# Kernel tuning notes

Measured on AMD Instinct MI355X. Metric: run time of the kernel, lower is better.

## Reference

```python
import jax, jax.numpy as jnp
import numpy as np

B, IN, O, F, FH = 512, 2000, 64, 8, 32
D = 64 + FH * O  # 2112


def setup_inputs() -> dict:
    key = jax.random.key(0)
    ks = jax.random.split(key, 17)
    rn = lambda k, s: jax.random.normal(k, s, dtype=jnp.float32) * 0.05
    return dict(
        x=rn(ks[0], (B, IN)),
        fc_in_W=rn(ks[1], (1024, IN)), fc_in_b=rn(ks[2], (1024,)),
        fc1_W=rn(ks[3], (128, 1024)), fc1_b=rn(ks[4], (128,)),
        out1_W=rn(ks[5], (O, 64, 128)), out1_b=rn(ks[6], (O, 64)),
        coef_nn_W=rn(ks[7], (F, FH, 1)), coef_nn_b=rn(ks[8], (F, FH)),
        coef_att_W=rn(ks[9], (F, FH, FH)),
        out_att_W=rn(ks[10], (O, FH, FH)),
        nodes_trans_W=rn(ks[11], (O, O)),
        trans_gcn_W=rn(ks[12], (D, D)),
        outmap_W=rn(ks[13], (1, D)), outmap_b=rn(ks[14], (1,)),
        prelu_a=jnp.float32(0.25),
        coef_m=rn(ks[15], (O, O, F)),
    )


def reference(x, fc_in_W, fc_in_b, fc1_W, fc1_b, out1_W, out1_b,
              coef_nn_W, coef_nn_b, coef_att_W, out_att_W,
              nodes_trans_W, trans_gcn_W, outmap_W, outmap_b, prelu_a, coef_m):
    elu = jax.nn.elu
    # trunk MLP
    h = jax.nn.relu(x @ fc_in_W.T + fc_in_b)          # [B,1024]
    h = jax.nn.relu(h @ fc1_W.T + fc1_b)              # [B,128]
    # per-output-node heads (vectorized over the output_dim loop)
    hiddens = jax.nn.relu(jnp.einsum('bk,odk->bod', h, out1_W) + out1_b)  # [B,O,64]
    # per-feature coef embedding: Linear(1,FH) on each coef_m[:,:,i] slice
    cf = elu(coef_m[..., None] * coef_nn_W[:, :, 0] + coef_nn_b)          # [O,O,F,FH]
    # sum over concatenated feature axis (F*FH) of exp(elu(.))
    s = jnp.exp(elu(cf)).sum(axis=(2, 3))[:, :, None, None]               # [O,O,1,1]
    lin = jnp.einsum('xyfh,fgh->xyfg', cf, coef_att_W)                    # per-feature attention linear
    p = elu(jnp.exp(elu(cf)) * lin / s)
    cfs = elu(p.sum(axis=2) / F)                                          # [O,O,FH]
    # node-level attention (vectorized over the output_dim loop)
    coef_sum = jnp.exp(elu(cfs)).sum(axis=1)                              # [O,FH]
    p2 = jnp.exp(elu(cfs)) / coef_sum[:, None, :]                         # [O,O,FH]
    lin2 = jnp.einsum('oih,igh->oig', cfs, out_att_W)
    att = (p2 * lin2).reshape(O, O * FH)                                  # concat over i (i-major)
    hc = jnp.concatenate(
        [hiddens, jnp.broadcast_to(att[None], (x.shape[0], O, O * FH))], axis=2)  # [B,O,D]
    nt = jnp.einsum('bpd,op->bod', hc, nodes_trans_W)                     # node mixing Linear(O,O)
    trans = jax.nn.sigmoid(jnp.einsum('bod,ed->boe', nt, trans_gcn_W))    # [B,O,D]
    z = (trans @ outmap_W.T + outmap_b).squeeze(-1)                       # [B,O]
    return jnp.where(z >= 0, z, prelu_a * z)                              # PReLU
```

## Files before the change

kernel.cpp:

```cpp
#include <hip/hip_runtime.h>
#include <math.h>

typedef __attribute__((ext_vector_type(8))) short bf16x8;
typedef __attribute__((ext_vector_type(4))) float f32x4;

static __device__ __forceinline__ float fast_elu(float x) {
    return x > 0.0f ? x : __expf(x) - 1.0f;
}

static __device__ __forceinline__ unsigned short f2bf(float f) {
    unsigned int u = __float_as_uint(f);
    unsigned int r = (u + 0x7FFFu + ((u >> 16) & 1u)) >> 16;
    return (unsigned short)r;
}

static __device__ __forceinline__ bf16x8 cvt8(const float* __restrict__ s) {
    float4 a = *reinterpret_cast<const float4*>(s);
    float4 b = *reinterpret_cast<const float4*>(s + 4);
    bf16x8 r;
    r[0] = (short)f2bf(a.x); r[1] = (short)f2bf(a.y);
    r[2] = (short)f2bf(a.z); r[3] = (short)f2bf(a.w);
    r[4] = (short)f2bf(b.x); r[5] = (short)f2bf(b.y);
    r[6] = (short)f2bf(b.z); r[7] = (short)f2bf(b.w);
    return r;
}

#define T0 16384
#define T1 16896
#define T2 82432
#define T3 99328
#define CONV_BLOCKS 388

static __device__ __forceinline__ void conv_phase(
    int bx,
    const float* __restrict__ fc1W, const float* __restrict__ ntW,
    const float* __restrict__ out1W, const float* __restrict__ tgw,
    unsigned short* __restrict__ fc1Wb, unsigned short* __restrict__ Wb,
    unsigned short* __restrict__ out1WbT, unsigned short* __restrict__ Gb)
{
    int u = bx * 256 + threadIdx.x;
    if (u < T0) {
        int i8 = u * 8;
        *reinterpret_cast<bf16x8*>(&fc1Wb[i8]) = cvt8(&fc1W[i8]);
    } else if (u < T1) {
        int i8 = (u - T0) * 8;
        *reinterpret_cast<bf16x8*>(&Wb[i8]) = cvt8(&ntW[i8]);
    } else if (u < T2) {
        int i = u - T1;
        int n = i >> 4, kc = i & 15;
        int d = n >> 6, p = n & 63;
        *reinterpret_cast<bf16x8*>(&out1WbT[(size_t)n * 128 + kc * 8]) =
            cvt8(&out1W[(size_t)((p << 6) | d) * 128 + kc * 8]);
    } else if (u < T3) {
        int i = u - T2;
        int e = i >> 3, c = i & 7;
        *reinterpret_cast<bf16x8*>(&Gb[(size_t)e * 64 + c * 8]) =
            cvt8(&tgw[(size_t)e * 2112 + c * 8]);
    }
}

static __device__ __forceinline__ void coef_phase(
    int bx, float* __restrict__ smemf,
    const float* __restrict__ coef_m, const float* __restrict__ cW,
    const float* __restrict__ cB, const float* __restrict__ attW,
    float* __restrict__ cfs)
{
    float* cf_s = smemf;
    float* part = smemf + 1024;
    const int t = threadIdx.x;
    const int wv = t >> 6, lane = t & 63;
    const int xy = bx * 4 + wv;
    float ls = 0.0f;
    #pragma unroll
    for (int i = 0; i < 4; ++i) {
        int idx = i * 64 + lane;
        int f = idx >> 5;
        float v = fast_elu(coef_m[xy * 8 + f] * cW[idx] + cB[idx]);
        cf_s[wv * 256 + idx] = v;
        ls += __expf(fast_elu(v));
    }
    #pragma unroll
    for (int m = 1; m < 64; m <<= 1) ls += __shfl_xor(ls, m, 64);
    __syncthreads();
    const float rs = __builtin_amdgcn_rcpf(ls);
    const int g = lane & 31, fg = lane >> 5;
    float acc = 0.0f;
    for (int f = fg * 4; f < fg * 4 + 4; ++f) {
        float lin = 0.0f;
        #pragma unroll
        for (int h = 0; h < 32; h += 4) {
            float4 Lv = *reinterpret_cast<const float4*>(&cf_s[wv * 256 + f * 32 + h]);
            float4 Wv = *reinterpret_cast<const float4*>(&attW[f * 1024 + g * 32 + h]);
            lin += Lv.x * Wv.x + Lv.y * Wv.y + Lv.z * Wv.z + Lv.w * Wv.w;
        }
        float e = __expf(fast_elu(cf_s[wv * 256 + f * 32 + g]));
        acc += fast_elu(e * lin * rs);
    }
    part[wv * 64 + lane] = acc;
    __syncthreads();
    if (lane < 32) {
        float tot = part[wv * 64 + lane] + part[wv * 64 + lane + 32];
        cfs[xy * 32 + lane] = fast_elu(tot * 0.125f);
    }
}

static __device__ __forceinline__ void att_phase(
    int o, int ic, float* __restrict__ smemf,
    const float* __restrict__ cfs, const float* __restrict__ oattW,
    float* __restrict__ att)
{
    float* L    = smemf;
    float* red  = smemf + 2048;
    float* csum = smemf + 2304;
    const int t = threadIdx.x;
    #pragma unroll
    for (int j = 0; j < 8; ++j) L[t + 256 * j] = cfs[o * 2048 + t + 256 * j];
    __syncthreads();
    {
        int h = t & 31, ig = t >> 5;
        float ps = 0.0f;
        for (int i = ig * 8; i < ig * 8 + 8; ++i) ps += __expf(fast_elu(L[i * 32 + h]));
        red[t] = ps;
        __syncthreads();
        if (t < 32) {
            float cs = 0.0f;
            #pragma unroll
            for (int j = 0; j < 8; ++j) cs += red[j * 32 + t];
            csum[t] = cs;
        }
        __syncthreads();
    }
    int idx = ic * 256 + t;
    int i = idx >> 5, g = idx & 31;
    float lin2 = 0.0f;
    #pragma unroll
    for (int h = 0; h < 32; h += 4) {
        float4 Lv = *reinterpret_cast<const float4*>(&L[i * 32 + h]);
        float4 Wv = *reinterpret_cast<const float4*>(&oattW[i * 1024 + g * 32 + h]);
        lin2 += Lv.x * Wv.x + Lv.y * Wv.y + Lv.z * Wv.z + Lv.w * Wv.w;
    }
    float p2 = __expf(fast_elu(L[idx])) * __builtin_amdgcn_rcpf(csum[g]);
    att[o * 2048 + idx] = p2 * lin2;
}

static __device__ __forceinline__ void natt_phase(
    int bx, float* __restrict__ smemf,
    const float* __restrict__ ntW, const float* __restrict__ att,
    unsigned short* __restrict__ nattb)
{
    float* ntW_s = smemf;
    float* att_s = smemf + 64 * 65;
    const int t = threadIdx.x;
    const int d0 = bx * 16;
    #pragma unroll
    for (int j = 0; j < 16; ++j) {
        int idx = t + 256 * j;
        ntW_s[(idx >> 6) * 65 + (idx & 63)] = ntW[idx];
    }
    #pragma unroll
    for (int j = 0; j < 4; ++j) {
        int idx = t + 256 * j;
        int p = idx >> 4, dd = idx & 15;
        att_s[p * 17 + dd] = att[p * 2048 + d0 + dd];
    }
    __syncthreads();
    const int dd = t & 15, ob = (t >> 4) * 4;
    float acc[4] = {0.0f, 0.0f, 0.0f, 0.0f};
    for (int p = 0; p < 64; ++p) {
        float av = att_s[p * 17 + dd];
        #pragma unroll
        for (int i = 0; i < 4; ++i) acc[i] += ntW_s[(ob + i) * 65 + p] * av;
    }
    #pragma unroll
    for (int i = 0; i < 4; ++i)
        nattb[(ob + i) * 2048 + d0 + dd] = f2bf(acc[i]);
}

static __device__ __forceinline__ void gemm_core(
    const unsigned short* __restrict__ A, int lda,
    const unsigned short* __restrict__ B, int ldb,
    float* __restrict__ C, int ldc, long strideCz,
    int kchunk, int bn, int bm, int bz,
    unsigned short* __restrict__ As, unsigned short* __restrict__ Bs)
{
    const int t = threadIdx.x;
    const int w = t >> 6, lane = t & 63, l16 = lane & 15, quad = lane >> 4;
    const int n0 = bn * 64, m0 = bm * 64;
    const int kb0 = bz * kchunk;
    const int r = t >> 2, koff = (t & 3) * 8;
    C += (size_t)bz * strideCz;

    const size_t arow = (size_t)(m0 + r) * lda + koff;
    const size_t brow = (size_t)(n0 + r) * ldb + koff;
    bf16x8 av = *reinterpret_cast<const bf16x8*>(&A[arow + kb0]);
    bf16x8 bv = *reinterpret_cast<const bf16x8*>(&B[brow + kb0]);

    f32x4 acc[4] = {};
    for (int kb = kb0; kb < kb0 + kchunk; kb += 32) {
        __syncthreads();
        *reinterpret_cast<bf16x8*>(&As[r * 40 + koff]) = av;
        *reinterpret_cast<bf16x8*>(&Bs[r * 40 + koff]) = bv;
        if (kb + 32 < kb0 + kchunk) {
            av = *reinterpret_cast<const bf16x8*>(&A[arow + kb + 32]);
            bv = *reinterpret_cast<const bf16x8*>(&B[brow + kb + 32]);
        }
        __syncthreads();
        bf16x8 af = *reinterpret_cast<const bf16x8*>(&As[(w * 16 + l16) * 40 + quad * 8]);
        #pragma unroll
        for (int nt = 0; nt < 4; ++nt) {
            bf16x8 bf = *reinterpret_cast<const bf16x8*>(&Bs[(nt * 16 + l16) * 40 + quad * 8]);
            acc[nt] = __builtin_amdgcn_mfma_f32_16x16x32_bf16(af, bf, acc[nt], 0, 0, 0);
        }
    }
    #pragma unroll
    for (int nt = 0; nt < 4; ++nt)
        #pragma unroll
        for (int i = 0; i < 4; ++i) {
            int m = m0 + w * 16 + quad * 4 + i;
            int n = n0 + nt * 16 + l16;
            C[(size_t)m * ldc + n] = acc[nt][i];
        }
}

static __device__ __forceinline__ void gemm_xf_core(
    const float* __restrict__ A, const float* __restrict__ B,
    const float* __restrict__ bias, unsigned short* __restrict__ Cb,
    int bn, int bm,
    unsigned short* __restrict__ As, unsigned short* __restrict__ Bs)
{
    const int t = threadIdx.x;
    const int w = t >> 6, lane = t & 63, l16 = lane & 15, quad = lane >> 4;
    const int n0 = bn * 64, m0 = bm * 64;
    const int r = t >> 2, koff = (t & 3) * 8;

    const float* arow = A + (size_t)(m0 + r) * 2000;
    const float* brow = B + (size_t)(n0 + r) * 2000;
    const bf16x8 zv = {0, 0, 0, 0, 0, 0, 0, 0};

    bf16x8 av = (koff < 2000) ? cvt8(arow + koff) : zv;
    bf16x8 bv = (koff < 2000) ? cvt8(brow + koff) : zv;

    f32x4 acc[4] = {};
    for (int kb = 0; kb < 2000; kb += 32) {
        __syncthreads();
        *reinterpret_cast<bf16x8*>(&As[r * 40 + koff]) = av;
        *reinterpret_cast<bf16x8*>(&Bs[r * 40 + koff]) = bv;
        if (kb + 32 < 2000) {
            int k = kb + 32 + koff;
            av = (k < 2000) ? cvt8(arow + k) : zv;
            bv = (k < 2000) ? cvt8(brow + k) : zv;
        }
        __syncthreads();
        bf16x8 af = *reinterpret_cast<const bf16x8*>(&As[(w * 16 + l16) * 40 + quad * 8]);
        #pragma unroll
        for (int nt = 0; nt < 4; ++nt) {
            bf16x8 bf = *reinterpret_cast<const bf16x8*>(&Bs[(nt * 16 + l16) * 40 + quad * 8]);
            acc[nt] = __builtin_amdgcn_mfma_f32_16x16x32_bf16(af, bf, acc[nt], 0, 0, 0);
        }
    }
    #pragma unroll
    for (int nt = 0; nt < 4; ++nt)
        #pragma unroll
        for (int i = 0; i < 4; ++i) {
            int m = m0 + w * 16 + quad * 4 + i;
            int n = n0 + nt * 16 + l16;
            float v = acc[nt][i] + bias[n];
            v = fmaxf(v, 0.0f);
            Cb[(size_t)m * 1024 + n] = f2bf(v);
        }
}

static __device__ __forceinline__ void gemm_tgwa_core(
    const float* __restrict__ tgw,
    const unsigned short* __restrict__ B,
    float* __restrict__ C, long strideCz,
    int kchunk, int bm, int bz,
    unsigned short* __restrict__ As, unsigned short* __restrict__ Bs)
{
    const int t = threadIdx.x;
    const int w = t >> 6, lane = t & 63, l16 = lane & 15, quad = lane >> 4;
    const int m0 = bm * 64;
    const int kb0 = bz * kchunk;
    const int r = t >> 2, koff = (t & 3) * 8;
    C += (size_t)bz * strideCz;

    const float* arow = tgw + (size_t)(m0 + r) * 2112 + 64 + koff;
    const unsigned short* brow = B + (size_t)r * 2048 + koff;
    bf16x8 av = cvt8(arow + kb0);
    bf16x8 bv = *reinterpret_cast<const bf16x8*>(brow + kb0);

    f32x4 acc[4] = {};
    for (int kb = kb0; kb < kb0 + kchunk; kb += 32) {
        __syncthreads();
        *reinterpret_cast<bf16x8*>(&As[r * 40 + koff]) = av;
        *reinterpret_cast<bf16x8*>(&Bs[r * 40 + koff]) = bv;
        if (kb + 32 < kb0 + kchunk) {
            av = cvt8(arow + kb + 32);
            bv = *reinterpret_cast<const bf16x8*>(brow + kb + 32);
        }
        __syncthreads();
        bf16x8 af = *reinterpret_cast<const bf16x8*>(&As[(w * 16 + l16) * 40 + quad * 8]);
        #pragma unroll
        for (int nt = 0; nt < 4; ++nt) {
            bf16x8 bf = *reinterpret_cast<const bf16x8*>(&Bs[(nt * 16 + l16) * 40 + quad * 8]);
            acc[nt] = __builtin_amdgcn_mfma_f32_16x16x32_bf16(af, bf, acc[nt], 0, 0, 0);
        }
    }
    #pragma unroll
    for (int nt = 0; nt < 4; ++nt)
        #pragma unroll
        for (int i = 0; i < 4; ++i) {
            int m = m0 + w * 16 + quad * 4 + i;
            int n = nt * 16 + l16;
            C[(size_t)m * 64 + n] = acc[nt][i];
        }
}

static __device__ __forceinline__ void gemm_fa_core(
    const float* __restrict__ Ap, int lda, long apstride, int nparts,
    const float* __restrict__ abias,
    const unsigned short* __restrict__ B, int ldb,
    unsigned short* __restrict__ Cb, int ldc,
    const float* __restrict__ bias,
    int kchunk, int bn, int bm,
    unsigned short* __restrict__ As, unsigned short* __restrict__ Bs)
{
    const int t = threadIdx.x;
    const int w = t >> 6, lane = t & 63, l16 = lane & 15, quad = lane >> 4;
    const int n0 = bn * 64, m0 = bm * 64;
    const int r = t >> 2, koff = (t & 3) * 8;

    f32x4 acc[4] = {};
    for (int kb = 0; kb < kchunk; kb += 32) {
        float a8[8];
        {
            const float* base = &Ap[(size_t)(m0 + r) * lda + kb + koff];
            float4 s0 = *reinterpret_cast<const float4*>(base);
            float4 s1 = *reinterpret_cast<const float4*>(base + 4);
            for (int j = 1; j < nparts; ++j) {
                const float* pj = base + (size_t)j * apstride;
                float4 p0 = *reinterpret_cast<const float4*>(pj);
                float4 p1 = *reinterpret_cast<const float4*>(pj + 4);
                s0.x += p0.x; s0.y += p0.y; s0.z += p0.z; s0.w += p0.w;
                s1.x += p1.x; s1.y += p1.y; s1.z += p1.z; s1.w += p1.w;
            }
            float4 b0 = *reinterpret_cast<const float4*>(&abias[kb + koff]);
            float4 b1 = *reinterpret_cast<const float4*>(&abias[kb + koff + 4]);
            a8[0] = fmaxf(s0.x + b0.x, 0.0f); a8[1] = fmaxf(s0.y + b0.y, 0.0f);
            a8[2] = fmaxf(s0.z + b0.z, 0.0f); a8[3] = fmaxf(s0.w + b0.w, 0.0f);
            a8[4] = fmaxf(s1.x + b1.x, 0.0f); a8[5] = fmaxf(s1.y + b1.y, 0.0f);
            a8[6] = fmaxf(s1.z + b1.z, 0.0f); a8[7] = fmaxf(s1.w + b1.w, 0.0f);
        }
        bf16x8 bv = *reinterpret_cast<const bf16x8*>(&B[(size_t)(n0 + r) * ldb + kb + koff]);
        __syncthreads();
        ushort4 lo, hi;
        lo.x = f2bf(a8[0]); lo.y = f2bf(a8[1]); lo.z = f2bf(a8[2]); lo.w = f2bf(a8[3]);
        hi.x = f2bf(a8[4]); hi.y = f2bf(a8[5]); hi.z = f2bf(a8[6]); hi.w = f2bf(a8[7]);
        *reinterpret_cast<ushort4*>(&As[r * 40 + koff]) = lo;
        *reinterpret_cast<ushort4*>(&As[r * 40 + koff + 4]) = hi;
        *reinterpret_cast<bf16x8*>(&Bs[r * 40 + koff]) = bv;
        __syncthreads();
        bf16x8 af = *reinterpret_cast<const bf16x8*>(&As[(w * 16 + l16) * 40 + quad * 8]);
        #pragma unroll
        for (int nt = 0; nt < 4; ++nt) {
            bf16x8 bf = *reinterpret_cast<const bf16x8*>(&Bs[(nt * 16 + l16) * 40 + quad * 8]);
            acc[nt] = __builtin_amdgcn_mfma_f32_16x16x32_bf16(af, bf, acc[nt], 0, 0, 0);
        }
    }
    #pragma unroll
    for (int nt = 0; nt < 4; ++nt)
        #pragma unroll
        for (int i = 0; i < 4; ++i) {
            int m = m0 + w * 16 + quad * 4 + i;
            int n = n0 + nt * 16 + l16;
            int bidx = (((n & 63) << 6) | (n >> 6));
            float v = acc[nt][i] + bias[bidx];
            v = fmaxf(v, 0.0f);
            Cb[(size_t)m * ldc + n] = f2bf(v);
        }
}

static __device__ __forceinline__ void nt1f_phase(
    int b, unsigned short* __restrict__ smemu,
    const unsigned short* __restrict__ hbT, const unsigned short* __restrict__ Wb,
    unsigned short* __restrict__ nt1b)
{
    unsigned short* HtT   = smemu;
    unsigned short* nt1_s = smemu + 64 * 72;
    const int t = threadIdx.x;
    const int w = t >> 6, lane = t & 63, l16 = lane & 15, quad = lane >> 4;

    const unsigned short* src = hbT + (size_t)b * 4096;
    #pragma unroll
    for (int j = 0; j < 2; ++j) {
        int c = t + j * 256;
        *reinterpret_cast<bf16x8*>(&HtT[(c >> 3) * 72 + (c & 7) * 8]) =
            *reinterpret_cast<const bf16x8*>(&src[c * 8]);
    }
    __syncthreads();

    bf16x8 aW[2];
    #pragma unroll
    for (int h = 0; h < 2; ++h)
        aW[h] = *reinterpret_cast<const bf16x8*>(&Wb[(w * 16 + l16) * 64 + h * 32 + quad * 8]);
    #pragma unroll
    for (int dt = 0; dt < 4; ++dt) {
        f32x4 acc = {0.0f, 0.0f, 0.0f, 0.0f};
        #pragma unroll
        for (int h = 0; h < 2; ++h) {
            bf16x8 bf = *reinterpret_cast<const bf16x8*>(
                &HtT[(dt * 16 + l16) * 72 + h * 32 + quad * 8]);
            acc = __builtin_amdgcn_mfma_f32_16x16x32_bf16(aW[h], bf, acc, 0, 0, 0);
        }
        #pragma unroll
        for (int i = 0; i < 4; ++i)
            nt1_s[(w * 16 + quad * 4 + i) * 72 + dt * 16 + l16] = f2bf(acc[i]);
    }
    __syncthreads();
    #pragma unroll
    for (int j = 0; j < 2; ++j) {
        int c = t + j * 256;
        *reinterpret_cast<bf16x8*>(&nt1b[(size_t)b * 4096 + c * 8]) =
            *reinterpret_cast<const bf16x8*>(&nt1_s[(c >> 3) * 72 + (c & 7) * 8]);
    }
}

__global__ __launch_bounds__(256) void uber1(
    const float* fc1W, const float* ntW, const float* out1W, const float* tgw,
    unsigned short* fc1Wb, unsigned short* Wb, unsigned short* out1WbT,
    unsigned short* Gb,
    const float* coef_m, const float* cW, const float* cB, const float* attW,
    float* cfs)
{
    __shared__ __align__(16) float smemf[1280];
    int bx = blockIdx.x;
    if (bx < CONV_BLOCKS)
        conv_phase(bx, fc1W, ntW, out1W, tgw, fc1Wb, Wb, out1WbT, Gb);
    else
        coef_phase(bx - CONV_BLOCKS, smemf, coef_m, cW, cB, attW, cfs);
}

__global__ __launch_bounds__(256) void uber2(
    const float* x, const float* fcinW, const float* fc_in_b,
    unsigned short* h1b,
    const float* cfs, const float* oattW, float* att)
{
    __shared__ __align__(16) float smemf[2592];
    int bx = blockIdx.x;
    if (bx < 128) {
        unsigned short* As = (unsigned short*)smemf;
        gemm_xf_core(x, fcinW, fc_in_b, h1b, bx & 15, bx >> 4, As, As + 2560);
    } else {
        int b2 = bx - 128;
        att_phase(b2 & 63, b2 >> 6, smemf, cfs, oattW, att);
    }
}

__global__ __launch_bounds__(256) void uber3(
    const unsigned short* h1b, const unsigned short* fc1Wb, float* h2p,
    const float* ntW, const float* att, unsigned short* nattb)
{
    __shared__ __align__(16) float smemf[5248];
    int bx = blockIdx.x;
    if (bx < 64) {
        unsigned short* As = (unsigned short*)smemf;
        gemm_core(h1b, 1024, fc1Wb, 1024, h2p, 128, 65536L,
                  256, bx & 1, (bx >> 1) & 7, bx >> 4, As, As + 2560);
    } else {
        natt_phase(bx - 64, smemf, ntW, att, nattb);
    }
}

__global__ __launch_bounds__(256) void uber4(
    const float* h2p, const float* fc1_b, const unsigned short* out1WbT,
    unsigned short* hbT, const float* out1_b,
    const float* tgw, const unsigned short* nattb, float* cpT)
{
    __shared__ __align__(16) float smemf[2560];
    unsigned short* As = (unsigned short*)smemf;
    int bx = blockIdx.x;
    if (bx < 512) {
        gemm_fa_core(h2p, 128, 65536L, 4, fc1_b, out1WbT, 128,
                     hbT, 4096, out1_b, 128, bx & 63, bx >> 6, As, As + 2560);
    } else {
        int b2 = bx - 512;
        gemm_tgwa_core(tgw, nattb, cpT, 135168L, 256,
                       b2 % 33, b2 / 33, As, As + 2560);
    }
}

__global__ __launch_bounds__(256) void uber5(
    const unsigned short* hbT, const unsigned short* Wb, unsigned short* nt1b,
    const float* cpT, float* cmatT)
{
    __shared__ __align__(16) unsigned short smemu[2 * 64 * 72];
    int bx = blockIdx.x;
    if (bx < 512) {
        nt1f_phase(bx, smemu, hbT, Wb, nt1b);
    } else {
        int i = (bx - 512) * 256 + threadIdx.x;
        if (i < 135168) {
            float a = 0.0f;
            #pragma unroll
            for (int j = 0; j < 8; ++j) a += cpT[i + (long)j * 135168L];
            cmatT[i] = a;
        }
    }
}

__global__ __launch_bounds__(256) void final_nb(
    const unsigned short* __restrict__ nt1b,
    const unsigned short* __restrict__ Gb,
    const float* __restrict__ cmatT,
    const float* __restrict__ outW,
    float* __restrict__ zpart)
{
    const int t = threadIdx.x;
    const int w = t >> 6, lane = t & 63, l16 = lane & 15, quad = lane >> 4;
    const int eb = blockIdx.x;
    const int b0 = blockIdx.y * 16;
    const int o = w * 16 + l16;

    bf16x8 ga[4][2];
    float cm[4][4], wv[4][4];
    #pragma unroll
    for (int et = 0; et < 4; ++et) {
        #pragma unroll
        for (int h = 0; h < 2; ++h)
            ga[et][h] = *reinterpret_cast<const bf16x8*>(
                &Gb[(size_t)(eb * 64 + et * 16 + l16) * 64 + h * 32 + quad * 8]);
        #pragma unroll
        for (int i = 0; i < 4; ++i) {
            int e = eb * 64 + et * 16 + quad * 4 + i;
            cm[et][i] = cmatT[(size_t)e * 64 + o];
            wv[et][i] = outW[e];
        }
    }

    const unsigned short* bbase = nt1b + (size_t)b0 * 4096 + o * 64 + quad * 8;
    bf16x8 bf0 = *reinterpret_cast<const bf16x8*>(bbase);
    bf16x8 bf1 = *reinterpret_cast<const bf16x8*>(bbase + 32);

    for (int bi = 0; bi < 16; ++bi) {
        bf16x8 nb0, nb1;
        if (bi < 15) {
            nb0 = *reinterpret_cast<const bf16x8*>(bbase + (size_t)(bi + 1) * 4096);
            nb1 = *reinterpret_cast<const bf16x8*>(bbase + (size_t)(bi + 1) * 4096 + 32);
        }
        float zo = 0.0f;
        #pragma unroll
        for (int et = 0; et < 4; ++et) {
            f32x4 acc = {cm[et][0], cm[et][1], cm[et][2], cm[et][3]};
            acc = __builtin_amdgcn_mfma_f32_16x16x32_bf16(ga[et][0], bf0, acc, 0, 0, 0);
            acc = __builtin_amdgcn_mfma_f32_16x16x32_bf16(ga[et][1], bf1, acc, 0, 0, 0);
            #pragma unroll
            for (int i = 0; i < 4; ++i)
                zo += __builtin_amdgcn_rcpf(1.0f + __expf(-acc[i])) * wv[et][i];
        }
        zo += __shfl_xor(zo, 16, 64);
        zo += __shfl_xor(zo, 32, 64);
        if (quad == 0)
            zpart[((size_t)eb * 512 + b0 + bi) * 64 + o] = zo;
        bf0 = nb0; bf1 = nb1;
    }
}

__global__ __launch_bounds__(256) void finish_kernel(
    const float* __restrict__ zpart, const float* __restrict__ outB,
    const float* __restrict__ preluA, float* __restrict__ out)
{
    int i = blockIdx.x * 256 + threadIdx.x;
    float z = 0.0f;
    for (int j = 0; j < 33; ++j) z += zpart[(size_t)j * 32768 + i];
    z += outB[0];
    float pa = preluA[0];
    out[i] = (z >= 0.0f) ? z : pa * z;
}

extern "C" void kernel_launch(void* const* d_in, const int* in_sizes, int n_in,
                              void* d_out, int out_size, void* d_ws, size_t ws_size,
                              hipStream_t stream)
{
    const float* x       = (const float*)d_in[0];
    const float* fc_in_W = (const float*)d_in[1];
    const float* fc_in_b = (const float*)d_in[2];
    const float* fc1_W   = (const float*)d_in[3];
    const float* fc1_b   = (const float*)d_in[4];
    const float* out1_W  = (const float*)d_in[5];
    const float* out1_b  = (const float*)d_in[6];
    const float* cW      = (const float*)d_in[7];
    const float* cB      = (const float*)d_in[8];
    const float* cattW   = (const float*)d_in[9];
    const float* oattW   = (const float*)d_in[10];
    const float* ntW     = (const float*)d_in[11];
    const float* tgw     = (const float*)d_in[12];
    const float* outW    = (const float*)d_in[13];
    const float* outB    = (const float*)d_in[14];
    const float* preluA  = (const float*)d_in[15];
    const float* coef_m  = (const float*)d_in[16];
    float* out = (float*)d_out;
    float* ws  = (float*)d_ws;

    unsigned short* fc1Wb   = (unsigned short*)(ws + 0);
    unsigned short* Wb      = (unsigned short*)(ws + 65536);
    unsigned short* out1WbT = (unsigned short*)(ws + 67584);
    unsigned short* Gb      = (unsigned short*)(ws + 329728);
    float*          cfs     = ws + 397312;
    float*          att     = ws + 528384;
    unsigned short* nattb   = (unsigned short*)(ws + 659456);
    unsigned short* h1b     = (unsigned short*)(ws + 724992);
    float*          h2p     = ws + 987136;
    unsigned short* hbT     = (unsigned short*)(ws + 1249280);
    float*          cpT     = ws + 2297856;
    float*          cmatT   = ws + 3379200;
    unsigned short* nt1b    = (unsigned short*)(ws + 3514368);
    float*          zpart   = ws + 4562944;

    uber1<<<CONV_BLOCKS + 1024, 256, 0, stream>>>(
        fc1_W, ntW, out1_W, tgw, fc1Wb, Wb, out1WbT, Gb,
        coef_m, cW, cB, cattW, cfs);
    uber2<<<640, 256, 0, stream>>>(x, fc_in_W, fc_in_b, h1b, cfs, oattW, att);
    uber3<<<192, 256, 0, stream>>>(h1b, fc1Wb, h2p, ntW, att, nattb);
    uber4<<<776, 256, 0, stream>>>(h2p, fc1_b, out1WbT, hbT, out1_b,
                                   tgw, nattb, cpT);
    uber5<<<1040, 256, 0, stream>>>(hbT, Wb, nt1b, cpT, cmatT);
    final_nb<<<dim3(33, 32), 256, 0, stream>>>(nt1b, Gb, cmatT, outW, zpart);
    finish_kernel<<<128, 256, 0, stream>>>(zpart, outB, preluA, out);
}
```

Before: 234.2 us.

## Split-K the input GEMM across four chunks and fuse the reduction into fc1

The first GEMM (x @ fc_in_W.T, K=2000) previously ran as 128 blocks, each looping over the full K. It now splits K into four 512-wide chunks, giving 512 blocks that write fp32 partials. The next GEMM sums the four partials, adds the bias and applies ReLU while loading its A operand, reusing the generalized gemm_fa_core. This raises parallelism on a long-K GEMM that underfilled the GPU. The cost is extra fp32 partial traffic and a larger workspace.

```diff
diff --git a/kernel.cpp b/kernel.cpp
--- a/kernel.cpp
+++ b/kernel.cpp
@@ -176,33 +176,35 @@
         nattb[(ob + i) * 2048 + d0 + dd] = f2bf(acc[i]);
 }
 
-static __device__ __forceinline__ void gemm_core(
-    const unsigned short* __restrict__ A, int lda,
-    const unsigned short* __restrict__ B, int ldb,
+static __device__ __forceinline__ void gemm_xfs_core(
+    const float* __restrict__ A, const float* __restrict__ B,
     float* __restrict__ C, int ldc, long strideCz,
-    int kchunk, int bn, int bm, int bz,
+    int bn, int bm, int bz,
     unsigned short* __restrict__ As, unsigned short* __restrict__ Bs)
 {
     const int t = threadIdx.x;
     const int w = t >> 6, lane = t & 63, l16 = lane & 15, quad = lane >> 4;
     const int n0 = bn * 64, m0 = bm * 64;
-    const int kb0 = bz * kchunk;
+    const int kb0 = bz * 512;
     const int r = t >> 2, koff = (t & 3) * 8;
     C += (size_t)bz * strideCz;
 
-    const size_t arow = (size_t)(m0 + r) * lda + koff;
-    const size_t brow = (size_t)(n0 + r) * ldb + koff;
-    bf16x8 av = *reinterpret_cast<const bf16x8*>(&A[arow + kb0]);
-    bf16x8 bv = *reinterpret_cast<const bf16x8*>(&B[brow + kb0]);
+    const float* arow = A + (size_t)(m0 + r) * 2000;
+    const float* brow = B + (size_t)(n0 + r) * 2000;
+    const bf16x8 zv = {0, 0, 0, 0, 0, 0, 0, 0};
+    int k0 = kb0 + koff;
+    bf16x8 av = (k0 < 2000) ? cvt8(arow + k0) : zv;
+    bf16x8 bv = (k0 < 2000) ? cvt8(brow + k0) : zv;
 
     f32x4 acc[4] = {};
-    for (int kb = kb0; kb < kb0 + kchunk; kb += 32) {
+    for (int kb = kb0; kb < kb0 + 512; kb += 32) {
         __syncthreads();
         *reinterpret_cast<bf16x8*>(&As[r * 40 + koff]) = av;
         *reinterpret_cast<bf16x8*>(&Bs[r * 40 + koff]) = bv;
-        if (kb + 32 < kb0 + kchunk) {
-            av = *reinterpret_cast<const bf16x8*>(&A[arow + kb + 32]);
-            bv = *reinterpret_cast<const bf16x8*>(&B[brow + kb + 32]);
+        if (kb + 32 < kb0 + 512) {
+            int k = kb + 32 + koff;
+            av = (k < 2000) ? cvt8(arow + k) : zv;
+            bv = (k < 2000) ? cvt8(brow + k) : zv;
         }
         __syncthreads();
         bf16x8 af = *reinterpret_cast<const bf16x8*>(&As[(w * 16 + l16) * 40 + quad * 8]);
@@ -219,54 +221,6 @@
             int m = m0 + w * 16 + quad * 4 + i;
             int n = n0 + nt * 16 + l16;
             C[(size_t)m * ldc + n] = acc[nt][i];
-        }
-}
-
-static __device__ __forceinline__ void gemm_xf_core(
-    const float* __restrict__ A, const float* __restrict__ B,
-    const float* __restrict__ bias, unsigned short* __restrict__ Cb,
-    int bn, int bm,
-    unsigned short* __restrict__ As, unsigned short* __restrict__ Bs)
-{
-    const int t = threadIdx.x;
-    const int w = t >> 6, lane = t & 63, l16 = lane & 15, quad = lane >> 4;
-    const int n0 = bn * 64, m0 = bm * 64;
-    const int r = t >> 2, koff = (t & 3) * 8;
-
-    const float* arow = A + (size_t)(m0 + r) * 2000;
-    const float* brow = B + (size_t)(n0 + r) * 2000;
-    const bf16x8 zv = {0, 0, 0, 0, 0, 0, 0, 0};
-
-    bf16x8 av = (koff < 2000) ? cvt8(arow + koff) : zv;
-    bf16x8 bv = (koff < 2000) ? cvt8(brow + koff) : zv;
-
-    f32x4 acc[4] = {};
-    for (int kb = 0; kb < 2000; kb += 32) {
-        __syncthreads();
-        *reinterpret_cast<bf16x8*>(&As[r * 40 + koff]) = av;
-        *reinterpret_cast<bf16x8*>(&Bs[r * 40 + koff]) = bv;
-        if (kb + 32 < 2000) {
-            int k = kb + 32 + koff;
-            av = (k < 2000) ? cvt8(arow + k) : zv;
-            bv = (k < 2000) ? cvt8(brow + k) : zv;
-        }
-        __syncthreads();
-        bf16x8 af = *reinterpret_cast<const bf16x8*>(&As[(w * 16 + l16) * 40 + quad * 8]);
-        #pragma unroll
-        for (int nt = 0; nt < 4; ++nt) {
-            bf16x8 bf = *reinterpret_cast<const bf16x8*>(&Bs[(nt * 16 + l16) * 40 + quad * 8]);
-            acc[nt] = __builtin_amdgcn_mfma_f32_16x16x32_bf16(af, bf, acc[nt], 0, 0, 0);
-        }
-    }
-    #pragma unroll
-    for (int nt = 0; nt < 4; ++nt)
-        #pragma unroll
-        for (int i = 0; i < 4; ++i) {
-            int m = m0 + w * 16 + quad * 4 + i;
-            int n = n0 + nt * 16 + l16;
-            float v = acc[nt][i] + bias[n];
-            v = fmaxf(v, 0.0f);
-            Cb[(size_t)m * 1024 + n] = f2bf(v);
         }
 }
 
@@ -320,18 +274,20 @@
     const float* __restrict__ Ap, int lda, long apstride, int nparts,
     const float* __restrict__ abias,
     const unsigned short* __restrict__ B, int ldb,
-    unsigned short* __restrict__ Cb, int ldc,
-    const float* __restrict__ bias,
-    int kchunk, int bn, int bm,
+    float* __restrict__ C, unsigned short* __restrict__ Cb,
+    int ldc, long strideCz, const float* __restrict__ bias,
+    int mode, int kchunk, int bn, int bm, int bz,
     unsigned short* __restrict__ As, unsigned short* __restrict__ Bs)
 {
     const int t = threadIdx.x;
     const int w = t >> 6, lane = t & 63, l16 = lane & 15, quad = lane >> 4;
     const int n0 = bn * 64, m0 = bm * 64;
+    const int kb0 = bz * kchunk;
     const int r = t >> 2, koff = (t & 3) * 8;
+    if (mode == 0) C += (size_t)bz * strideCz;
 
     f32x4 acc[4] = {};
-    for (int kb = 0; kb < kchunk; kb += 32) {
+    for (int kb = kb0; kb < kb0 + kchunk; kb += 32) {
         float a8[8];
         {
             const float* base = &Ap[(size_t)(m0 + r) * lda + kb + koff];
@@ -373,10 +329,14 @@
         for (int i = 0; i < 4; ++i) {
             int m = m0 + w * 16 + quad * 4 + i;
             int n = n0 + nt * 16 + l16;
-            int bidx = (((n & 63) << 6) | (n >> 6));
-            float v = acc[nt][i] + bias[bidx];
-            v = fmaxf(v, 0.0f);
-            Cb[(size_t)m * ldc + n] = f2bf(v);
+            if (mode == 0) {
+                C[(size_t)m * ldc + n] = acc[nt][i];
+            } else {
+                int bidx = (((n & 63) << 6) | (n >> 6));
+                float v = acc[nt][i] + bias[bidx];
+                v = fmaxf(v, 0.0f);
+                Cb[(size_t)m * ldc + n] = f2bf(v);
+            }
         }
 }
 
@@ -441,31 +401,33 @@
 }
 
 __global__ __launch_bounds__(256) void uber2(
-    const float* x, const float* fcinW, const float* fc_in_b,
-    unsigned short* h1b,
+    const float* x, const float* fcinW, float* h1p,
     const float* cfs, const float* oattW, float* att)
 {
     __shared__ __align__(16) float smemf[2592];
     int bx = blockIdx.x;
-    if (bx < 128) {
+    if (bx < 512) {
         unsigned short* As = (unsigned short*)smemf;
-        gemm_xf_core(x, fcinW, fc_in_b, h1b, bx & 15, bx >> 4, As, As + 2560);
+        gemm_xfs_core(x, fcinW, h1p, 1024, 524288L,
+                      bx & 15, (bx >> 4) & 7, bx >> 7, As, As + 2560);
     } else {
-        int b2 = bx - 128;
+        int b2 = bx - 512;
         att_phase(b2 & 63, b2 >> 6, smemf, cfs, oattW, att);
     }
 }
 
 __global__ __launch_bounds__(256) void uber3(
-    const unsigned short* h1b, const unsigned short* fc1Wb, float* h2p,
+    const float* h1p, const float* fc_in_b, const unsigned short* fc1Wb,
+    float* h2p,
     const float* ntW, const float* att, unsigned short* nattb)
 {
     __shared__ __align__(16) float smemf[5248];
     int bx = blockIdx.x;
     if (bx < 64) {
         unsigned short* As = (unsigned short*)smemf;
-        gemm_core(h1b, 1024, fc1Wb, 1024, h2p, 128, 65536L,
-                  256, bx & 1, (bx >> 1) & 7, bx >> 4, As, As + 2560);
+        gemm_fa_core(h1p, 1024, 524288L, 4, fc_in_b, fc1Wb, 1024,
+                     h2p, nullptr, 128, 65536L, nullptr, 0, 256,
+                     bx & 1, (bx >> 1) & 7, bx >> 4, As, As + 2560);
     } else {
         natt_phase(bx - 64, smemf, ntW, att, nattb);
     }
@@ -481,7 +443,8 @@
     int bx = blockIdx.x;
     if (bx < 512) {
         gemm_fa_core(h2p, 128, 65536L, 4, fc1_b, out1WbT, 128,
-                     hbT, 4096, out1_b, 128, bx & 63, bx >> 6, As, As + 2560);
+                     nullptr, hbT, 4096, 0L, out1_b, 2, 128,
+                     bx & 63, bx >> 6, 0, As, As + 2560);
     } else {
         int b2 = bx - 512;
         gemm_tgwa_core(tgw, nattb, cpT, 135168L, 256,
@@ -608,19 +571,19 @@
     float*          cfs     = ws + 397312;
     float*          att     = ws + 528384;
     unsigned short* nattb   = (unsigned short*)(ws + 659456);
-    unsigned short* h1b     = (unsigned short*)(ws + 724992);
-    float*          h2p     = ws + 987136;
-    unsigned short* hbT     = (unsigned short*)(ws + 1249280);
-    float*          cpT     = ws + 2297856;
-    float*          cmatT   = ws + 3379200;
-    unsigned short* nt1b    = (unsigned short*)(ws + 3514368);
-    float*          zpart   = ws + 4562944;
+    float*          h1p     = ws + 724992;
+    float*          h2p     = ws + 2822144;
+    unsigned short* hbT     = (unsigned short*)(ws + 3084288);
+    float*          cpT     = ws + 4132864;
+    float*          cmatT   = ws + 5214208;
+    unsigned short* nt1b    = (unsigned short*)(ws + 5349376);
+    float*          zpart   = ws + 6397952;
 
     uber1<<<CONV_BLOCKS + 1024, 256, 0, stream>>>(
         fc1_W, ntW, out1_W, tgw, fc1Wb, Wb, out1WbT, Gb,
         coef_m, cW, cB, cattW, cfs);
-    uber2<<<640, 256, 0, stream>>>(x, fc_in_W, fc_in_b, h1b, cfs, oattW, att);
-    uber3<<<192, 256, 0, stream>>>(h1b, fc1Wb, h2p, ntW, att, nattb);
+    uber2<<<1024, 256, 0, stream>>>(x, fc_in_W, h1p, cfs, oattW, att);
+    uber3<<<192, 256, 0, stream>>>(h1p, fc_in_b, fc1Wb, h2p, ntW, att, nattb);
     uber4<<<776, 256, 0, stream>>>(h2p, fc1_b, out1WbT, hbT, out1_b,
                                    tgw, nattb, cpT);
     uber5<<<1040, 256, 0, stream>>>(hbT, Wb, nt1b, cpT, cmatT);
```

Result: faster. 192.8 us (-17.7%).
